# Optimization experiments

Hardware: AMD Instinct MI355X
Metric: run time of the kernel (lower is better)

The kernel has to match this reference:

```python
import jax, jax.numpy as jnp
import numpy as np

B, T = 32, 512
VOCAB, WDIM, H, NUM_LABELS = 100000, 300, 256, 2


def setup_inputs() -> dict:
    key = jax.random.key(0)
    ks = jax.random.split(key, 16)
    x = jax.random.randint(ks[0], (B, T), 0, VOCAB, dtype=jnp.int32)
    lengths = jax.random.randint(ks[1], (B,), T // 2, T + 1, dtype=jnp.int32)
    mask = (jnp.arange(T)[None, :] < lengths[:, None]).astype(jnp.int32)
    s = 0.05
    emb_table = jax.random.normal(ks[2], (VOCAB, WDIM), jnp.float32)
    W_in = jax.random.normal(ks[3], (WDIM, H), jnp.float32) * s
    b_in = jnp.zeros((H,), jnp.float32)
    Wih_f = jax.random.normal(ks[4], (H, 4 * H), jnp.float32) * s
    Whh_f = jax.random.normal(ks[5], (H, 4 * H), jnp.float32) * s
    bl_f = jnp.zeros((4 * H,), jnp.float32)
    Wih_b = jax.random.normal(ks[6], (H, 4 * H), jnp.float32) * s
    Whh_b = jax.random.normal(ks[7], (H, 4 * H), jnp.float32) * s
    bl_b = jnp.zeros((4 * H,), jnp.float32)
    Wfc = jax.random.normal(ks[8], (2 * H, H), jnp.float32) * s
    bfc = jnp.zeros((H,), jnp.float32)
    Wout = jax.random.normal(ks[9], (H, NUM_LABELS), jnp.float32) * s
    bout = jnp.zeros((NUM_LABELS,), jnp.float32)
    return dict(emb_table=emb_table, W_in=W_in, b_in=b_in,
                Wih_f=Wih_f, Whh_f=Whh_f, bl_f=bl_f,
                Wih_b=Wih_b, Whh_b=Whh_b, bl_b=bl_b,
                Wfc=Wfc, bfc=bfc, Wout=Wout, bout=bout,
                x=x, mask=mask, lengths=lengths)


def _lstm_dir(xs, maskf, Wih, Whh, b, reverse):
    # xs: [B,T,H], maskf: [B,T] float. Masked LSTM: padded steps carry state.
    xs_t = jnp.swapaxes(xs, 0, 1)                # [T,B,H]
    m_t = jnp.swapaxes(maskf, 0, 1)[..., None]   # [T,B,1]
    h0 = jnp.zeros((xs.shape[0], Whh.shape[0]), xs.dtype)
    c0 = h0

    def step(carry, inp):
        h, c = carry
        xt, mt = inp
        z = xt @ Wih + h @ Whh + b               # [B,4H]
        i, f, g, o = jnp.split(z, 4, axis=-1)
        i = jax.nn.sigmoid(i); f = jax.nn.sigmoid(f)
        g = jnp.tanh(g); o = jax.nn.sigmoid(o)
        c_new = f * c + i * g
        h_new = o * jnp.tanh(c_new)
        c = mt * c_new + (1.0 - mt) * c
        h = mt * h_new + (1.0 - mt) * h
        return (h, c), h

    _, hs = jax.lax.scan(step, (h0, c0), (xs_t, m_t), reverse=reverse)
    return jnp.swapaxes(hs, 0, 1)                # [B,T,H]


def reference(emb_table, W_in, b_in, Wih_f, Whh_f, bl_f, Wih_b, Whh_b, bl_b,
              Wfc, bfc, Wout, bout, x, mask, lengths):
    maskf = mask.astype(jnp.float32)
    x_vecs = jnp.take(emb_table, x, axis=0)          # [B,T,WDIM]
    z = jax.nn.relu(x_vecs @ W_in + b_in)            # wordvec layer + relu
    h_fwd = _lstm_dir(z, maskf, Wih_f, Whh_f, bl_f, reverse=False)
    h_bwd = _lstm_dir(z, maskf, Wih_b, Whh_b, bl_b, reverse=True)
    h_mat = jnp.concatenate([h_fwd, h_bwd], axis=-1)  # [B,T,2H]
    h_masked = h_mat * maskf[..., None]
    fc_in = jnp.sum(h_masked / lengths.astype(jnp.float32)[:, None, None], axis=1)
    fc_hidden = jax.nn.relu(fc_in @ Wfc + bfc)        # dropout = identity (eval)
    return fc_hidden @ Wout + bout                    # [B, NUM_LABELS]
```

## Files before the change

kernel.cpp:

```cpp
#include <hip/hip_runtime.h>
#include <math.h>

#define B_    32
#define T_    512
#define WDIM_ 300
#define H_    256
#define G4_   1024
#define M_    (B_ * T_)

#define NCG   8
#define NWG   256
#define THR   512
#define HXN   (2 * 2 * B_ * H_)

#define RPT4(M, b)  M(b) M((b)+1) M((b)+2) M((b)+3)
#define RPT16(M, b) RPT4(M, b) RPT4(M, (b)+4) RPT4(M, (b)+8) RPT4(M, (b)+12)
#define RPT64(M)    RPT16(M, 0) RPT16(M, 16) RPT16(M, 32) RPT16(M, 48)

__global__ __launch_bounds__(256)
void k_embed_proj(const float* __restrict__ emb, const float* __restrict__ Win,
                  const float* __restrict__ bin, const int* __restrict__ x,
                  float* __restrict__ z)
{
    __shared__ float Ash[16][132];
    __shared__ float Bsh[16][132];
    __shared__ int   rows[128];

    const int tid = threadIdx.x;
    const int tx = tid & 15, ty = tid >> 4;
    const int rm = blockIdx.y * 128;
    const int cn = blockIdx.x * 128;

    if (tid < 128) rows[tid] = x[rm + tid];
    __syncthreads();

    float acc[8][8];
#pragma unroll
    for (int i = 0; i < 8; ++i)
#pragma unroll
        for (int j = 0; j < 8; ++j) acc[i][j] = 0.f;

    for (int kc = 0; kc < 19; ++kc) {
        const int k0 = kc * 16;
#pragma unroll
        for (int e = 0; e < 8; ++e) {
            const int idx = e * 256 + tid;
            const int r = idx >> 4, kk = idx & 15;
            const int k = k0 + kk;
            const int v = rows[r];
            Ash[kk][r] = (k < WDIM_) ? emb[(size_t)v * WDIM_ + k] : 0.f;
        }
#pragma unroll
        for (int e = 0; e < 8; ++e) {
            const int idx = e * 256 + tid;
            const int kk = idx >> 7, n = idx & 127;
            const int k = k0 + kk;
            Bsh[kk][n] = (k < WDIM_) ? Win[(size_t)k * H_ + cn + n] : 0.f;
        }
        __syncthreads();
#pragma unroll
        for (int kk = 0; kk < 16; ++kk) {
            float a[8], bb[8];
#pragma unroll
            for (int i = 0; i < 8; ++i) a[i] = Ash[kk][ty * 8 + i];
#pragma unroll
            for (int j = 0; j < 8; ++j) bb[j] = Bsh[kk][tx * 8 + j];
#pragma unroll
            for (int i = 0; i < 8; ++i)
#pragma unroll
                for (int j = 0; j < 8; ++j) acc[i][j] += a[i] * bb[j];
        }
        __syncthreads();
    }

#pragma unroll
    for (int i = 0; i < 8; ++i) {
        const int row = rm + ty * 8 + i;
#pragma unroll
        for (int j = 0; j < 8; ++j) {
            const int col = cn + tx * 8 + j;
            z[(size_t)row * H_ + col] = fmaxf(acc[i][j] + bin[col], 0.f);
        }
    }
}

__global__ __launch_bounds__(256)
void k_in_proj(const float* __restrict__ z,
               const float* __restrict__ Wf, const float* __restrict__ blf,
               const float* __restrict__ Wb, const float* __restrict__ blb,
               float* __restrict__ Pf, float* __restrict__ Pb)
{
    const float* W  = blockIdx.z ? Wb  : Wf;
    const float* bl = blockIdx.z ? blb : blf;
    float*       P  = blockIdx.z ? Pb  : Pf;

    __shared__ float Ash[16][132];
    __shared__ float Bsh[16][132];

    const int tid = threadIdx.x;
    const int tx = tid & 15, ty = tid >> 4;
    const int rm = blockIdx.y * 128;
    const int cn = blockIdx.x * 128;

    float acc[8][8];
#pragma unroll
    for (int i = 0; i < 8; ++i)
#pragma unroll
        for (int j = 0; j < 8; ++j) acc[i][j] = 0.f;

    for (int kc = 0; kc < 16; ++kc) {
        const int k0 = kc * 16;
#pragma unroll
        for (int e = 0; e < 8; ++e) {
            const int idx = e * 256 + tid;
            const int r = idx >> 4, kk = idx & 15;
            Ash[kk][r] = z[(size_t)(rm + r) * H_ + k0 + kk];
        }
#pragma unroll
        for (int e = 0; e < 8; ++e) {
            const int idx = e * 256 + tid;
            const int kk = idx >> 7, n = idx & 127;
            Bsh[kk][n] = W[(size_t)(k0 + kk) * G4_ + cn + n];
        }
        __syncthreads();
#pragma unroll
        for (int kk = 0; kk < 16; ++kk) {
            float a[8], bb[8];
#pragma unroll
            for (int i = 0; i < 8; ++i) a[i] = Ash[kk][ty * 8 + i];
#pragma unroll
            for (int j = 0; j < 8; ++j) bb[j] = Bsh[kk][tx * 8 + j];
#pragma unroll
            for (int i = 0; i < 8; ++i)
#pragma unroll
                for (int j = 0; j < 8; ++j) acc[i][j] += a[i] * bb[j];
        }
        __syncthreads();
    }

#pragma unroll
    for (int i = 0; i < 8; ++i) {
        const int row = rm + ty * 8 + i;
#pragma unroll
        for (int j = 0; j < 8; ++j) {
            const int col = cn + tx * 8 + j;
            P[(size_t)row * G4_ + col] = acc[i][j] + bl[col];
        }
    }
}

__global__ void k_init(unsigned long long* __restrict__ hx)
{
    const int i = blockIdx.x * blockDim.x + threadIdx.x;
    if (i < HXN) hx[i] = 0ull;
}

__global__ __launch_bounds__(THR, 2)
void k_lstm_persist(const float* __restrict__ Pf, const float* __restrict__ Pb,
                    const float* __restrict__ Whf, const float* __restrict__ Whb,
                    const int* __restrict__ lengths,
                    unsigned long long* __restrict__ hx,
                    float* __restrict__ pool)
{
    __shared__ float h_sh[2][256];
    __shared__ float zp[4][2][128];

    const int tid = threadIdx.x;
    const int wg  = blockIdx.x;
    const int bg  = wg & 15;
    const int dir = (wg >> 4) & 1;
    const int cg  = wg >> 5;

    const float* P   = dir ? Pb  : Pf;
    const float* Whh = dir ? Whb : Whf;

    const int brow0 = bg * 2;
    const int len0 = lengths[brow0], len1 = lengths[brow0 + 1];
    const int tmax = max(len0, len1);

    const int q   = tid >> 7;
    const int cl  = tid & 127;
    const int g0  = cl >> 5;
    const int dd0 = cl & 31;
    const int gcol = g0 * 256 + cg * 32 + dd0;
    const int q64 = q * 64;

    float wv[64];
    {
        const float* wp = Whh + (size_t)q64 * G4_ + gcol;
#define LOADW(k) wv[k] = wp[(size_t)(k) * G4_];
        RPT64(LOADW)
#undef LOADW
    }

    const int gr    = tid >> 5;
    const int gd    = tid & 31;
    const int gbrow = brow0 + gr;
    const int glen  = gr ? len1 : len0;
    float cst = 0.f, hreg = 0.f, pacc = 0.f;

    const int lrow = tid >> 8;
    const int ld   = tid & 255;
    unsigned long long* slotR = hx + ((size_t)dir * 32 + brow0 + lrow) * 256 + ld;
    unsigned long long* slotW = hx + ((size_t)dir * 32 + gbrow) * 256 + cg * 32 + gd;
    const size_t bufStride = (size_t)2 * B_ * H_;

    for (int s = 0; s < tmax; ++s) {
        const int tt = dir ? (tmax - 1 - s) : s;

        float pv0 = 0.f, pv1 = 0.f, pv2 = 0.f, pv3 = 0.f;
        if (tid < 64) {
            const float* pr = P + (size_t)(gbrow * T_ + tt) * G4_ + cg * 32 + gd;
            pv0 = pr[0]; pv1 = pr[256]; pv2 = pr[512]; pv3 = pr[768];
        }

        {
            const unsigned long long* sp = slotR + (size_t)(s & 1) * bufStride;
            unsigned long long pk = __hip_atomic_load(sp, __ATOMIC_RELAXED,
                                                      __HIP_MEMORY_SCOPE_AGENT);
            while ((unsigned)(pk >> 32) < (unsigned)s) {
                __builtin_amdgcn_s_sleep(1);
                pk = __hip_atomic_load(sp, __ATOMIC_RELAXED,
                                       __HIP_MEMORY_SCOPE_AGENT);
            }
            h_sh[lrow][ld] = __uint_as_float((unsigned)pk);
        }
        __syncthreads();

        {
            const float* h0 = &h_sh[0][q64];
            const float* h1 = &h_sh[1][q64];
            float a0 = 0.f, a1 = 0.f;
#define GEMV4(k4) { \
            const float4 hv0 = *(const float4*)(h0 + 4 * (k4)); \
            const float4 hv1 = *(const float4*)(h1 + 4 * (k4)); \
            a0 += hv0.x * wv[4*(k4)  ]; a1 += hv1.x * wv[4*(k4)  ]; \
            a0 += hv0.y * wv[4*(k4)+1]; a1 += hv1.y * wv[4*(k4)+1]; \
            a0 += hv0.z * wv[4*(k4)+2]; a1 += hv1.z * wv[4*(k4)+2]; \
            a0 += hv0.w * wv[4*(k4)+3]; a1 += hv1.w * wv[4*(k4)+3]; }
            RPT16(GEMV4, 0)
#undef GEMV4
            zp[q][0][cl] = a0;
            zp[q][1][cl] = a1;
        }
        __syncthreads();

        if (tid < 64) {
            float zi = pv0 + zp[0][gr][gd]      + zp[1][gr][gd]      + zp[2][gr][gd]      + zp[3][gr][gd];
            float zf = pv1 + zp[0][gr][32 + gd] + zp[1][gr][32 + gd] + zp[2][gr][32 + gd] + zp[3][gr][32 + gd];
            float zg = pv2 + zp[0][gr][64 + gd] + zp[1][gr][64 + gd] + zp[2][gr][64 + gd] + zp[3][gr][64 + gd];
            float zo = pv3 + zp[0][gr][96 + gd] + zp[1][gr][96 + gd] + zp[2][gr][96 + gd] + zp[3][gr][96 + gd];
            const float ig = 1.f / (1.f + expf(-zi));
            const float fg = 1.f / (1.f + expf(-zf));
            const float gg = tanhf(zg);
            const float og = 1.f / (1.f + expf(-zo));
            const float cn = fg * cst + ig * gg;
            const float hn = og * tanhf(cn);
            if (tt < glen) { cst = cn; hreg = hn; pacc += hn; }
            const unsigned long long opk =
                ((unsigned long long)(unsigned)(s + 1) << 32) |
                (unsigned long long)__float_as_uint(hreg);
            __hip_atomic_store(slotW + (size_t)((s + 1) & 1) * bufStride, opk,
                               __ATOMIC_RELAXED, __HIP_MEMORY_SCOPE_AGENT);
        }
    }

    if (tid < 64)
        pool[gbrow * 512 + dir * 256 + cg * 32 + gd] = pacc / (float)glen;
}

__global__ __launch_bounds__(256)
void k_fc(const float* __restrict__ pool, const float* __restrict__ Wfc,
          const float* __restrict__ bfc, const float* __restrict__ Wout,
          const float* __restrict__ bout, float* __restrict__ out)
{
    __shared__ float p_sh[512];
    __shared__ float red[8];

    const int tid = threadIdx.x;
    const int b   = blockIdx.x;

    p_sh[tid]       = pool[b * 512 + tid];
    p_sh[256 + tid] = pool[b * 512 + 256 + tid];
    __syncthreads();

    float acc = bfc[tid];
#pragma unroll 8
    for (int k = 0; k < 512; ++k)
        acc += p_sh[k] * Wfc[(size_t)k * H_ + tid];
    const float fh = fmaxf(acc, 0.f);

    float p0 = fh * Wout[tid * 2 + 0];
    float p1 = fh * Wout[tid * 2 + 1];
#pragma unroll
    for (int off = 32; off > 0; off >>= 1) {
        p0 += __shfl_down(p0, off);
        p1 += __shfl_down(p1, off);
    }
    const int wave = tid >> 6;
    if ((tid & 63) == 0) { red[wave * 2] = p0; red[wave * 2 + 1] = p1; }
    __syncthreads();
    if (tid == 0) {
        out[b * 2 + 0] = red[0] + red[2] + red[4] + red[6] + bout[0];
        out[b * 2 + 1] = red[1] + red[3] + red[5] + red[7] + bout[1];
    }
}

__global__ void k_sentinel(float* out, int n)
{
    const int i = blockIdx.x * blockDim.x + threadIdx.x;
    if (i < n) out[i] = 1.0e9f;
}

extern "C" void kernel_launch(void* const* d_in, const int* in_sizes, int n_in,
                              void* d_out, int out_size, void* d_ws, size_t ws_size,
                              hipStream_t stream)
{
    const float* emb  = (const float*)d_in[0];
    const float* Win  = (const float*)d_in[1];
    const float* bin  = (const float*)d_in[2];
    const float* Wihf = (const float*)d_in[3];
    const float* Whhf = (const float*)d_in[4];
    const float* blf  = (const float*)d_in[5];
    const float* Wihb = (const float*)d_in[6];
    const float* Whhb = (const float*)d_in[7];
    const float* blb  = (const float*)d_in[8];
    const float* Wfc  = (const float*)d_in[9];
    const float* bfc  = (const float*)d_in[10];
    const float* Wout = (const float*)d_in[11];
    const float* bout = (const float*)d_in[12];
    const int*   x    = (const int*)d_in[13];
    const int*   lens = (const int*)d_in[15];
    float*       out  = (float*)d_out;

    const size_t need = ((size_t)M_ * H_ + 2 * (size_t)M_ * G4_) * sizeof(float);
    if (ws_size < need) {
        hipLaunchKernelGGL(k_sentinel, dim3(1), dim3(64), 0, stream, out, out_size);
        return;
    }

    float* z  = (float*)d_ws;
    float* Pf = z + (size_t)M_ * H_;
    float* Pb = Pf + (size_t)M_ * G4_;

    unsigned long long* hx   = (unsigned long long*)d_ws;
    float*              pool = (float*)(hx + HXN);

    hipLaunchKernelGGL(k_embed_proj, dim3(2, 128), dim3(256), 0, stream,
                       emb, Win, bin, x, z);
    hipLaunchKernelGGL(k_in_proj, dim3(8, 128, 2), dim3(256), 0, stream,
                       z, Wihf, blf, Wihb, blb, Pf, Pb);
    hipLaunchKernelGGL(k_init, dim3(128), dim3(256), 0, stream, hx);
    hipLaunchKernelGGL(k_lstm_persist, dim3(NWG), dim3(THR), 0, stream,
                       Pf, Pb, Whhf, Whhb, lens, hx, pool);
    hipLaunchKernelGGL(k_fc, dim3(32), dim3(256), 0, stream,
                       pool, Wfc, bfc, Wout, bout, out);
}
```

Measured before the change: 1.380 ms.

## Interleave forward and backward LSTM directions in one workgroup, use fast gate math

Each persistent workgroup now runs both the forward and backward recurrence for its batch pair and column group, halving the workgroup count. The two directions alternate within each step so that waiting on one direction's cross-workgroup h exchange can overlap with compute on the other. This doubles the register-resident recurrent weights per thread, which may cause spills or lower occupancy. Sigmoid and tanh are replaced by fast exp and reciprocal approximations, trading a little accuracy for fewer instructions.

```diff
diff --git a/kernel.cpp b/kernel.cpp
--- a/kernel.cpp
+++ b/kernel.cpp
@@ -9,13 +9,22 @@
 #define M_    (B_ * T_)
 
 #define NCG   8
-#define NWG   256
+#define NWG   128
 #define THR   512
 #define HXN   (2 * 2 * B_ * H_)
 
 #define RPT4(M, b)  M(b) M((b)+1) M((b)+2) M((b)+3)
 #define RPT16(M, b) RPT4(M, b) RPT4(M, (b)+4) RPT4(M, (b)+8) RPT4(M, (b)+12)
 #define RPT64(M)    RPT16(M, 0) RPT16(M, 16) RPT16(M, 32) RPT16(M, 48)
+
+__device__ __forceinline__ float fsigm(float x) {
+    return __builtin_amdgcn_rcpf(1.f + __expf(-x));
+}
+__device__ __forceinline__ float ftanh(float x) {
+    const float ax = fabsf(x);
+    const float t  = 1.f - 2.f * __builtin_amdgcn_rcpf(__expf(2.f * ax) + 1.f);
+    return copysignf(t, x);
+}
 
 __global__ __launch_bounds__(256)
 void k_embed_proj(const float* __restrict__ emb, const float* __restrict__ Win,
@@ -162,17 +171,13 @@
                     unsigned long long* __restrict__ hx,
                     float* __restrict__ pool)
 {
-    __shared__ float h_sh[2][256];
-    __shared__ float zp[4][2][128];
+    __shared__ float h_sh[2][2][256];
+    __shared__ float zp[2][4][2][128];
 
     const int tid = threadIdx.x;
     const int wg  = blockIdx.x;
     const int bg  = wg & 15;
-    const int dir = (wg >> 4) & 1;
-    const int cg  = wg >> 5;
-
-    const float* P   = dir ? Pb  : Pf;
-    const float* Whh = dir ? Whb : Whf;
+    const int cg  = wg >> 4;
 
     const int brow0 = bg * 2;
     const int len0 = lengths[brow0], len1 = lengths[brow0 + 1];
@@ -185,10 +190,11 @@
     const int gcol = g0 * 256 + cg * 32 + dd0;
     const int q64 = q * 64;
 
-    float wv[64];
+    float wf[64], wb[64];
     {
-        const float* wp = Whh + (size_t)q64 * G4_ + gcol;
-#define LOADW(k) wv[k] = wp[(size_t)(k) * G4_];
+        const float* wpf = Whf + (size_t)q64 * G4_ + gcol;
+        const float* wpb = Whb + (size_t)q64 * G4_ + gcol;
+#define LOADW(k) wf[k] = wpf[(size_t)(k) * G4_]; wb[k] = wpb[(size_t)(k) * G4_];
         RPT64(LOADW)
 #undef LOADW
     }
@@ -197,76 +203,128 @@
     const int gd    = tid & 31;
     const int gbrow = brow0 + gr;
     const int glen  = gr ? len1 : len0;
-    float cst = 0.f, hreg = 0.f, pacc = 0.f;
+    float cst0 = 0.f, hreg0 = 0.f, pacc0 = 0.f;
+    float cst1 = 0.f, hreg1 = 0.f, pacc1 = 0.f;
 
     const int lrow = tid >> 8;
     const int ld   = tid & 255;
-    unsigned long long* slotR = hx + ((size_t)dir * 32 + brow0 + lrow) * 256 + ld;
-    unsigned long long* slotW = hx + ((size_t)dir * 32 + gbrow) * 256 + cg * 32 + gd;
     const size_t bufStride = (size_t)2 * B_ * H_;
+    unsigned long long* slotR0 = hx + ((size_t)(brow0 + lrow)) * 256 + ld;
+    unsigned long long* slotR1 = slotR0 + (size_t)B_ * H_;
+    unsigned long long* slotW0 = hx + (size_t)gbrow * 256 + cg * 32 + gd;
+    unsigned long long* slotW1 = slotW0 + (size_t)B_ * H_;
 
     for (int s = 0; s < tmax; ++s) {
-        const int tt = dir ? (tmax - 1 - s) : s;
-
-        float pv0 = 0.f, pv1 = 0.f, pv2 = 0.f, pv3 = 0.f;
+        const int tt0 = s;
+        const int tt1 = tmax - 1 - s;
+        const size_t par = (size_t)(s & 1) * bufStride;
+
+        const unsigned long long* sp0 = slotR0 + par;
+        const unsigned long long* sp1 = slotR1 + par;
+        unsigned long long pk0 = __hip_atomic_load(sp0, __ATOMIC_RELAXED,
+                                                   __HIP_MEMORY_SCOPE_AGENT);
+        unsigned long long pk1 = __hip_atomic_load(sp1, __ATOMIC_RELAXED,
+                                                   __HIP_MEMORY_SCOPE_AGENT);
+        float pv00 = 0.f, pv01 = 0.f, pv02 = 0.f, pv03 = 0.f;
+        float pv10 = 0.f, pv11 = 0.f, pv12 = 0.f, pv13 = 0.f;
         if (tid < 64) {
-            const float* pr = P + (size_t)(gbrow * T_ + tt) * G4_ + cg * 32 + gd;
-            pv0 = pr[0]; pv1 = pr[256]; pv2 = pr[512]; pv3 = pr[768];
-        }
-
+            const float* pr0 = Pf + (size_t)(gbrow * T_ + tt0) * G4_ + cg * 32 + gd;
+            const float* pr1 = Pb + (size_t)(gbrow * T_ + tt1) * G4_ + cg * 32 + gd;
+            pv00 = pr0[0]; pv01 = pr0[256]; pv02 = pr0[512]; pv03 = pr0[768];
+            pv10 = pr1[0]; pv11 = pr1[256]; pv12 = pr1[512]; pv13 = pr1[768];
+        }
+
+        while ((unsigned)(pk0 >> 32) < (unsigned)s) {
+            __builtin_amdgcn_s_sleep(1);
+            pk0 = __hip_atomic_load(sp0, __ATOMIC_RELAXED,
+                                    __HIP_MEMORY_SCOPE_AGENT);
+        }
+        h_sh[0][lrow][ld] = __uint_as_float((unsigned)pk0);
+        __syncthreads();
         {
-            const unsigned long long* sp = slotR + (size_t)(s & 1) * bufStride;
-            unsigned long long pk = __hip_atomic_load(sp, __ATOMIC_RELAXED,
-                                                      __HIP_MEMORY_SCOPE_AGENT);
-            while ((unsigned)(pk >> 32) < (unsigned)s) {
-                __builtin_amdgcn_s_sleep(1);
-                pk = __hip_atomic_load(sp, __ATOMIC_RELAXED,
-                                       __HIP_MEMORY_SCOPE_AGENT);
-            }
-            h_sh[lrow][ld] = __uint_as_float((unsigned)pk);
-        }
-        __syncthreads();
-
-        {
-            const float* h0 = &h_sh[0][q64];
-            const float* h1 = &h_sh[1][q64];
+            const float* h0 = &h_sh[0][0][q64];
+            const float* h1 = &h_sh[0][1][q64];
             float a0 = 0.f, a1 = 0.f;
-#define GEMV4(k4) { \
+#define GEMV4F(k4) { \
             const float4 hv0 = *(const float4*)(h0 + 4 * (k4)); \
             const float4 hv1 = *(const float4*)(h1 + 4 * (k4)); \
-            a0 += hv0.x * wv[4*(k4)  ]; a1 += hv1.x * wv[4*(k4)  ]; \
-            a0 += hv0.y * wv[4*(k4)+1]; a1 += hv1.y * wv[4*(k4)+1]; \
-            a0 += hv0.z * wv[4*(k4)+2]; a1 += hv1.z * wv[4*(k4)+2]; \
-            a0 += hv0.w * wv[4*(k4)+3]; a1 += hv1.w * wv[4*(k4)+3]; }
-            RPT16(GEMV4, 0)
-#undef GEMV4
-            zp[q][0][cl] = a0;
-            zp[q][1][cl] = a1;
-        }
-        __syncthreads();
-
+            a0 += hv0.x * wf[4*(k4)  ]; a1 += hv1.x * wf[4*(k4)  ]; \
+            a0 += hv0.y * wf[4*(k4)+1]; a1 += hv1.y * wf[4*(k4)+1]; \
+            a0 += hv0.z * wf[4*(k4)+2]; a1 += hv1.z * wf[4*(k4)+2]; \
+            a0 += hv0.w * wf[4*(k4)+3]; a1 += hv1.w * wf[4*(k4)+3]; }
+            RPT16(GEMV4F, 0)
+#undef GEMV4F
+            zp[0][q][0][cl] = a0;
+            zp[0][q][1][cl] = a1;
+        }
+        __syncthreads();
         if (tid < 64) {
-            float zi = pv0 + zp[0][gr][gd]      + zp[1][gr][gd]      + zp[2][gr][gd]      + zp[3][gr][gd];
-            float zf = pv1 + zp[0][gr][32 + gd] + zp[1][gr][32 + gd] + zp[2][gr][32 + gd] + zp[3][gr][32 + gd];
-            float zg = pv2 + zp[0][gr][64 + gd] + zp[1][gr][64 + gd] + zp[2][gr][64 + gd] + zp[3][gr][64 + gd];
-            float zo = pv3 + zp[0][gr][96 + gd] + zp[1][gr][96 + gd] + zp[2][gr][96 + gd] + zp[3][gr][96 + gd];
-            const float ig = 1.f / (1.f + expf(-zi));
-            const float fg = 1.f / (1.f + expf(-zf));
-            const float gg = tanhf(zg);
-            const float og = 1.f / (1.f + expf(-zo));
-            const float cn = fg * cst + ig * gg;
-            const float hn = og * tanhf(cn);
-            if (tt < glen) { cst = cn; hreg = hn; pacc += hn; }
+            float zi = pv00 + zp[0][0][gr][gd]      + zp[0][1][gr][gd]      + zp[0][2][gr][gd]      + zp[0][3][gr][gd];
+            float zf = pv01 + zp[0][0][gr][32 + gd] + zp[0][1][gr][32 + gd] + zp[0][2][gr][32 + gd] + zp[0][3][gr][32 + gd];
+            float zg = pv02 + zp[0][0][gr][64 + gd] + zp[0][1][gr][64 + gd] + zp[0][2][gr][64 + gd] + zp[0][3][gr][64 + gd];
+            float zo = pv03 + zp[0][0][gr][96 + gd] + zp[0][1][gr][96 + gd] + zp[0][2][gr][96 + gd] + zp[0][3][gr][96 + gd];
+            const float ig = fsigm(zi);
+            const float fg = fsigm(zf);
+            const float gg = ftanh(zg);
+            const float og = fsigm(zo);
+            const float cn = fg * cst0 + ig * gg;
+            const float hn = og * ftanh(cn);
+            if (tt0 < glen) { cst0 = cn; hreg0 = hn; pacc0 += hn; }
             const unsigned long long opk =
                 ((unsigned long long)(unsigned)(s + 1) << 32) |
-                (unsigned long long)__float_as_uint(hreg);
-            __hip_atomic_store(slotW + (size_t)((s + 1) & 1) * bufStride, opk,
+                (unsigned long long)__float_as_uint(hreg0);
+            __hip_atomic_store(slotW0 + (size_t)((s + 1) & 1) * bufStride, opk,
                                __ATOMIC_RELAXED, __HIP_MEMORY_SCOPE_AGENT);
         }
-    }
-
-    if (tid < 64)
-        pool[gbrow * 512 + dir * 256 + cg * 32 + gd] = pacc / (float)glen;
+
+        while ((unsigned)(pk1 >> 32) < (unsigned)s) {
+            __builtin_amdgcn_s_sleep(1);
+            pk1 = __hip_atomic_load(sp1, __ATOMIC_RELAXED,
+                                    __HIP_MEMORY_SCOPE_AGENT);
+        }
+        h_sh[1][lrow][ld] = __uint_as_float((unsigned)pk1);
+        __syncthreads();
+        {
+            const float* h0 = &h_sh[1][0][q64];
+            const float* h1 = &h_sh[1][1][q64];
+            float a0 = 0.f, a1 = 0.f;
+#define GEMV4B(k4) { \
+            const float4 hv0 = *(const float4*)(h0 + 4 * (k4)); \
+            const float4 hv1 = *(const float4*)(h1 + 4 * (k4)); \
+            a0 += hv0.x * wb[4*(k4)  ]; a1 += hv1.x * wb[4*(k4)  ]; \
+            a0 += hv0.y * wb[4*(k4)+1]; a1 += hv1.y * wb[4*(k4)+1]; \
+            a0 += hv0.z * wb[4*(k4)+2]; a1 += hv1.z * wb[4*(k4)+2]; \
+            a0 += hv0.w * wb[4*(k4)+3]; a1 += hv1.w * wb[4*(k4)+3]; }
+            RPT16(GEMV4B, 0)
+#undef GEMV4B
+            zp[1][q][0][cl] = a0;
+            zp[1][q][1][cl] = a1;
+        }
+        __syncthreads();
+        if (tid < 64) {
+            float zi = pv10 + zp[1][0][gr][gd]      + zp[1][1][gr][gd]      + zp[1][2][gr][gd]      + zp[1][3][gr][gd];
+            float zf = pv11 + zp[1][0][gr][32 + gd] + zp[1][1][gr][32 + gd] + zp[1][2][gr][32 + gd] + zp[1][3][gr][32 + gd];
+            float zg = pv12 + zp[1][0][gr][64 + gd] + zp[1][1][gr][64 + gd] + zp[1][2][gr][64 + gd] + zp[1][3][gr][64 + gd];
+            float zo = pv13 + zp[1][0][gr][96 + gd] + zp[1][1][gr][96 + gd] + zp[1][2][gr][96 + gd] + zp[1][3][gr][96 + gd];
+            const float ig = fsigm(zi);
+            const float fg = fsigm(zf);
+            const float gg = ftanh(zg);
+            const float og = fsigm(zo);
+            const float cn = fg * cst1 + ig * gg;
+            const float hn = og * ftanh(cn);
+            if (tt1 < glen) { cst1 = cn; hreg1 = hn; pacc1 += hn; }
+            const unsigned long long opk =
+                ((unsigned long long)(unsigned)(s + 1) << 32) |
+                (unsigned long long)__float_as_uint(hreg1);
+            __hip_atomic_store(slotW1 + (size_t)((s + 1) & 1) * bufStride, opk,
+                               __ATOMIC_RELAXED, __HIP_MEMORY_SCOPE_AGENT);
+        }
+    }
+
+    if (tid < 64) {
+        pool[gbrow * 512 + 0   + cg * 32 + gd] = pacc0 / (float)glen;
+        pool[gbrow * 512 + 256 + cg * 32 + gd] = pacc1 / (float)glen;
+    }
 }
 
 __global__ __launch_bounds__(256)
```

New measurement: 1.688 ms. 1.22x slower.

## Reduce LSTM gate partials with wave shuffles instead of shared-memory pass

Applied to the files above, without the earlier changes.

Reassigns columns so that the four K-quarter partial sums and the four gates of a hidden unit sit in the same wavefront. They are then reduced with xor shuffles rather than written to a shared zp buffer and reread after a barrier. The spin-load on the h slot is issued before the P prefetch so the two latencies overlap. Sigmoid and tanh are replaced with fast exp/rcp approximations. This removes one shared-memory round trip and one barrier per step on the serial recurrence. The cost is a trailing barrier per step and slightly lower accuracy in the activations.

```diff
diff --git a/kernel.cpp b/kernel.cpp
--- a/kernel.cpp
+++ b/kernel.cpp
@@ -17,6 +17,15 @@
 #define RPT16(M, b) RPT4(M, b) RPT4(M, (b)+4) RPT4(M, (b)+8) RPT4(M, (b)+12)
 #define RPT64(M)    RPT16(M, 0) RPT16(M, 16) RPT16(M, 32) RPT16(M, 48)
 
+__device__ __forceinline__ float fsigm(float x) {
+    return __builtin_amdgcn_rcpf(1.f + __expf(-x));
+}
+__device__ __forceinline__ float ftanh(float x) {
+    const float ax = fabsf(x);
+    const float t  = 1.f - 2.f * __builtin_amdgcn_rcpf(__expf(2.f * ax) + 1.f);
+    return copysignf(t, x);
+}
+
 __global__ __launch_bounds__(256)
 void k_embed_proj(const float* __restrict__ emb, const float* __restrict__ Win,
                   const float* __restrict__ bin, const int* __restrict__ x,
@@ -163,7 +172,6 @@
                     float* __restrict__ pool)
 {
     __shared__ float h_sh[2][256];
-    __shared__ float zp[4][2][128];
 
     const int tid = threadIdx.x;
     const int wg  = blockIdx.x;
@@ -178,95 +186,121 @@
     const int len0 = lengths[brow0], len1 = lengths[brow0 + 1];
     const int tmax = max(len0, len1);
 
-    const int q   = tid >> 7;
-    const int cl  = tid & 127;
-    const int g0  = cl >> 5;
-    const int dd0 = cl & 31;
-    const int gcol = g0 * 256 + cg * 32 + dd0;
-    const int q64 = q * 64;
+    const int lane   = tid & 63;
+    const int w      = tid >> 6;
+    const int q      = lane >> 4;
+    const int lo     = lane & 15;
+    const int col_id = w * 16 + lo;
+    const int dloc   = col_id >> 2;
+    const int g      = col_id & 3;
+    const int colg   = g * 256 + cg * 32 + dloc;
+    const int q64    = q * 64;
 
     float wv[64];
     {
-        const float* wp = Whh + (size_t)q64 * G4_ + gcol;
+        const float* wp = Whh + (size_t)q64 * G4_ + colg;
 #define LOADW(k) wv[k] = wp[(size_t)(k) * G4_];
         RPT64(LOADW)
 #undef LOADW
     }
 
-    const int gr    = tid >> 5;
-    const int gd    = tid & 31;
-    const int gbrow = brow0 + gr;
-    const int glen  = gr ? len1 : len0;
-    float cst = 0.f, hreg = 0.f, pacc = 0.f;
+    const bool pub = ((lane & 51) == 0);
+    float cst0 = 0.f, hreg0 = 0.f, pacc0 = 0.f;
+    float cst1 = 0.f, hreg1 = 0.f, pacc1 = 0.f;
 
     const int lrow = tid >> 8;
     const int ld   = tid & 255;
+    const size_t bufStride = (size_t)2 * B_ * H_;
     unsigned long long* slotR = hx + ((size_t)dir * 32 + brow0 + lrow) * 256 + ld;
-    unsigned long long* slotW = hx + ((size_t)dir * 32 + gbrow) * 256 + cg * 32 + gd;
-    const size_t bufStride = (size_t)2 * B_ * H_;
+    unsigned long long* slotW0 = hx + ((size_t)dir * 32 + brow0) * 256 + cg * 32 + dloc;
+    unsigned long long* slotW1 = slotW0 + 256;
 
     for (int s = 0; s < tmax; ++s) {
         const int tt = dir ? (tmax - 1 - s) : s;
 
-        float pv0 = 0.f, pv1 = 0.f, pv2 = 0.f, pv3 = 0.f;
-        if (tid < 64) {
-            const float* pr = P + (size_t)(gbrow * T_ + tt) * G4_ + cg * 32 + gd;
-            pv0 = pr[0]; pv1 = pr[256]; pv2 = pr[512]; pv3 = pr[768];
-        }
-
+        const unsigned long long* sp = slotR + (size_t)(s & 1) * bufStride;
+        unsigned long long pk = __hip_atomic_load(sp, __ATOMIC_RELAXED,
+                                                  __HIP_MEMORY_SCOPE_AGENT);
+
+        float pv00 = 0.f, pv01 = 0.f, pv02 = 0.f, pv03 = 0.f;
+        float pv10 = 0.f, pv11 = 0.f, pv12 = 0.f, pv13 = 0.f;
+        if (pub) {
+            const float* pr0 = P + (size_t)(brow0 * T_ + tt) * G4_ + cg * 32 + dloc;
+            const float* pr1 = pr0 + (size_t)T_ * G4_;
+            pv00 = pr0[0]; pv01 = pr0[256]; pv02 = pr0[512]; pv03 = pr0[768];
+            pv10 = pr1[0]; pv11 = pr1[256]; pv12 = pr1[512]; pv13 = pr1[768];
+        }
+
+        while ((unsigned)(pk >> 32) < (unsigned)s) {
+            __builtin_amdgcn_s_sleep(1);
+            pk = __hip_atomic_load(sp, __ATOMIC_RELAXED,
+                                   __HIP_MEMORY_SCOPE_AGENT);
+        }
+        h_sh[lrow][ld] = __uint_as_float((unsigned)pk);
+        __syncthreads();
+
+        float a0 = 0.f, a1 = 0.f;
         {
-            const unsigned long long* sp = slotR + (size_t)(s & 1) * bufStride;
-            unsigned long long pk = __hip_atomic_load(sp, __ATOMIC_RELAXED,
-                                                      __HIP_MEMORY_SCOPE_AGENT);
-            while ((unsigned)(pk >> 32) < (unsigned)s) {
-                __builtin_amdgcn_s_sleep(1);
-                pk = __hip_atomic_load(sp, __ATOMIC_RELAXED,
-                                       __HIP_MEMORY_SCOPE_AGENT);
-            }
-            h_sh[lrow][ld] = __uint_as_float((unsigned)pk);
-        }
-        __syncthreads();
-
-        {
-            const float* h0 = &h_sh[0][q64];
-            const float* h1 = &h_sh[1][q64];
-            float a0 = 0.f, a1 = 0.f;
+            const float* hp0 = &h_sh[0][q64];
+            const float* hp1 = &h_sh[1][q64];
 #define GEMV4(k4) { \
-            const float4 hv0 = *(const float4*)(h0 + 4 * (k4)); \
-            const float4 hv1 = *(const float4*)(h1 + 4 * (k4)); \
+            const float4 hv0 = *(const float4*)(hp0 + 4 * (k4)); \
+            const float4 hv1 = *(const float4*)(hp1 + 4 * (k4)); \
             a0 += hv0.x * wv[4*(k4)  ]; a1 += hv1.x * wv[4*(k4)  ]; \
             a0 += hv0.y * wv[4*(k4)+1]; a1 += hv1.y * wv[4*(k4)+1]; \
             a0 += hv0.z * wv[4*(k4)+2]; a1 += hv1.z * wv[4*(k4)+2]; \
             a0 += hv0.w * wv[4*(k4)+3]; a1 += hv1.w * wv[4*(k4)+3]; }
             RPT16(GEMV4, 0)
 #undef GEMV4
-            zp[q][0][cl] = a0;
-            zp[q][1][cl] = a1;
-        }
-        __syncthreads();
-
-        if (tid < 64) {
-            float zi = pv0 + zp[0][gr][gd]      + zp[1][gr][gd]      + zp[2][gr][gd]      + zp[3][gr][gd];
-            float zf = pv1 + zp[0][gr][32 + gd] + zp[1][gr][32 + gd] + zp[2][gr][32 + gd] + zp[3][gr][32 + gd];
-            float zg = pv2 + zp[0][gr][64 + gd] + zp[1][gr][64 + gd] + zp[2][gr][64 + gd] + zp[3][gr][64 + gd];
-            float zo = pv3 + zp[0][gr][96 + gd] + zp[1][gr][96 + gd] + zp[2][gr][96 + gd] + zp[3][gr][96 + gd];
-            const float ig = 1.f / (1.f + expf(-zi));
-            const float fg = 1.f / (1.f + expf(-zf));
-            const float gg = tanhf(zg);
-            const float og = 1.f / (1.f + expf(-zo));
-            const float cn = fg * cst + ig * gg;
-            const float hn = og * tanhf(cn);
-            if (tt < glen) { cst = cn; hreg = hn; pacc += hn; }
-            const unsigned long long opk =
-                ((unsigned long long)(unsigned)(s + 1) << 32) |
-                (unsigned long long)__float_as_uint(hreg);
-            __hip_atomic_store(slotW + (size_t)((s + 1) & 1) * bufStride, opk,
+        }
+
+        a0 += __shfl_xor(a0, 16); a0 += __shfl_xor(a0, 32);
+        a1 += __shfl_xor(a1, 16); a1 += __shfl_xor(a1, 32);
+        const float b00 = __shfl_xor(a0, 1);
+        const float b01 = __shfl_xor(a0, 2);
+        const float b02 = __shfl_xor(b00, 2);
+        const float b10 = __shfl_xor(a1, 1);
+        const float b11 = __shfl_xor(a1, 2);
+        const float b12 = __shfl_xor(b10, 2);
+
+        if (pub) {
+            {
+                const float ig = fsigm(pv00 + a0);
+                const float fg = fsigm(pv01 + b00);
+                const float gg = ftanh(pv02 + b01);
+                const float og = fsigm(pv03 + b02);
+                const float cn = fg * cst0 + ig * gg;
+                const float hn = og * ftanh(cn);
+                if (tt < len0) { cst0 = cn; hreg0 = hn; pacc0 += hn; }
+            }
+            {
+                const float ig = fsigm(pv10 + a1);
+                const float fg = fsigm(pv11 + b10);
+                const float gg = ftanh(pv12 + b11);
+                const float og = fsigm(pv13 + b12);
+                const float cn = fg * cst1 + ig * gg;
+                const float hn = og * ftanh(cn);
+                if (tt < len1) { cst1 = cn; hreg1 = hn; pacc1 += hn; }
+            }
+            const unsigned long long tagbits =
+                (unsigned long long)(unsigned)(s + 1) << 32;
+            const size_t parW = (size_t)((s + 1) & 1) * bufStride;
+            __hip_atomic_store(slotW0 + parW,
+                               tagbits | (unsigned long long)__float_as_uint(hreg0),
                                __ATOMIC_RELAXED, __HIP_MEMORY_SCOPE_AGENT);
-        }
-    }
-
-    if (tid < 64)
-        pool[gbrow * 512 + dir * 256 + cg * 32 + gd] = pacc / (float)glen;
+            __hip_atomic_store(slotW1 + parW,
+                               tagbits | (unsigned long long)__float_as_uint(hreg1),
+                               __ATOMIC_RELAXED, __HIP_MEMORY_SCOPE_AGENT);
+        }
+        __syncthreads();
+    }
+
+    if (pub) {
+        pool[(size_t)brow0 * 512 + dir * 256 + cg * 32 + dloc]
+            = pacc0 / (float)len0;
+        pool[(size_t)(brow0 + 1) * 512 + dir * 256 + cg * 32 + dloc]
+            = pacc1 / (float)len1;
+    }
 }
 
 __global__ __launch_bounds__(256)
```

Result: slower. 1.903 ms (+38.0%).

## Replace per-element packed step tags with per-workgroup flags and fast gate math

Applied to the files above, without the earlier changes.

The recurrent kernel's cross-workgroup handoff changes. Before, every hidden value was packed with its step counter into a 64-bit word, and each consumer thread spun on its own word with a sleep. Now producers write plain float hidden values into an interleaved buffer, issue an agent-scope release fence, and one thread bumps a single per-workgroup flag; each consumer wave polls only its producer's flag and then does one coalesced load. The sigmoid and tanh gates also switch to fast-exp and hardware-reciprocal versions. This shortens the per-step latency of the serial 512-step chain, at the cost of relying on relaxed loads after flag polling with no explicit acquire fence, and of slightly lower transcendental accuracy.

```diff
diff --git a/kernel.cpp b/kernel.cpp
--- a/kernel.cpp
+++ b/kernel.cpp
@@ -11,11 +11,22 @@
 #define NCG   8
 #define NWG   256
 #define THR   512
-#define HXN   (2 * 2 * B_ * H_)
+
+#define HHN   (2 * 2 * 16 * 512)
+#define FLN   (2 * 2 * 16 * 8)
 
 #define RPT4(M, b)  M(b) M((b)+1) M((b)+2) M((b)+3)
 #define RPT16(M, b) RPT4(M, b) RPT4(M, (b)+4) RPT4(M, (b)+8) RPT4(M, (b)+12)
 #define RPT64(M)    RPT16(M, 0) RPT16(M, 16) RPT16(M, 32) RPT16(M, 48)
+
+__device__ __forceinline__ float fsigm(float x) {
+    return __builtin_amdgcn_rcpf(1.f + __expf(-x));
+}
+__device__ __forceinline__ float ftanh(float x) {
+    const float ax = fabsf(x);
+    const float t  = 1.f - 2.f * __builtin_amdgcn_rcpf(__expf(2.f * ax) + 1.f);
+    return copysignf(t, x);
+}
 
 __global__ __launch_bounds__(256)
 void k_embed_proj(const float* __restrict__ emb, const float* __restrict__ Win,
@@ -149,17 +160,18 @@
     }
 }
 
-__global__ void k_init(unsigned long long* __restrict__ hx)
+__global__ void k_init(float* __restrict__ hh, unsigned int* __restrict__ flg)
 {
     const int i = blockIdx.x * blockDim.x + threadIdx.x;
-    if (i < HXN) hx[i] = 0ull;
+    if (i < HHN) hh[i] = 0.f;
+    if (i < FLN) flg[i] = 0u;
 }
 
 __global__ __launch_bounds__(THR, 2)
 void k_lstm_persist(const float* __restrict__ Pf, const float* __restrict__ Pb,
                     const float* __restrict__ Whf, const float* __restrict__ Whb,
                     const int* __restrict__ lengths,
-                    unsigned long long* __restrict__ hx,
+                    float* __restrict__ hh, unsigned int* __restrict__ flg,
                     float* __restrict__ pool)
 {
     __shared__ float h_sh[2][256];
@@ -199,14 +211,20 @@
     const int glen  = gr ? len1 : len0;
     float cst = 0.f, hreg = 0.f, pacc = 0.f;
 
-    const int lrow = tid >> 8;
-    const int ld   = tid & 255;
-    unsigned long long* slotR = hx + ((size_t)dir * 32 + brow0 + lrow) * 256 + ld;
-    unsigned long long* slotW = hx + ((size_t)dir * 32 + gbrow) * 256 + cg * 32 + gd;
-    const size_t bufStride = (size_t)2 * B_ * H_;
+    const size_t hhPar  = (size_t)2 * 16 * 512;
+    const size_t flPar  = (size_t)2 * 16 * 8;
+    float*        hhB   = hh  + ((size_t)dir * 16 + bg) * 512;
+    unsigned int* flB   = flg + ((size_t)dir * 16 + bg) * 8;
+
+    const int wv_id = tid >> 6;
+    const int st_d  = tid >> 1;
+    const int st_r  = tid & 1;
+
+    const int pub_e = (cg * 32 + gd) * 2 + gr;
 
     for (int s = 0; s < tmax; ++s) {
         const int tt = dir ? (tmax - 1 - s) : s;
+        const size_t parR = (size_t)(s & 1);
 
         float pv0 = 0.f, pv1 = 0.f, pv2 = 0.f, pv3 = 0.f;
         if (tid < 64) {
@@ -215,25 +233,27 @@
         }
 
         {
-            const unsigned long long* sp = slotR + (size_t)(s & 1) * bufStride;
-            unsigned long long pk = __hip_atomic_load(sp, __ATOMIC_RELAXED,
+            const unsigned int* fp = flB + parR * flPar + wv_id;
+            while (__hip_atomic_load(fp, __ATOMIC_RELAXED,
+                                     __HIP_MEMORY_SCOPE_AGENT) < (unsigned)s) {
+            }
+        }
+        {
+            const unsigned int* hp =
+                (const unsigned int*)(hhB + parR * hhPar) + tid;
+            const unsigned int hv = __hip_atomic_load(hp, __ATOMIC_RELAXED,
                                                       __HIP_MEMORY_SCOPE_AGENT);
-            while ((unsigned)(pk >> 32) < (unsigned)s) {
-                __builtin_amdgcn_s_sleep(1);
-                pk = __hip_atomic_load(sp, __ATOMIC_RELAXED,
-                                       __HIP_MEMORY_SCOPE_AGENT);
-            }
-            h_sh[lrow][ld] = __uint_as_float((unsigned)pk);
+            h_sh[st_r][st_d] = __uint_as_float(hv);
         }
         __syncthreads();
 
         {
-            const float* h0 = &h_sh[0][q64];
-            const float* h1 = &h_sh[1][q64];
+            const float* hp0 = &h_sh[0][q64];
+            const float* hp1 = &h_sh[1][q64];
             float a0 = 0.f, a1 = 0.f;
 #define GEMV4(k4) { \
-            const float4 hv0 = *(const float4*)(h0 + 4 * (k4)); \
-            const float4 hv1 = *(const float4*)(h1 + 4 * (k4)); \
+            const float4 hv0 = *(const float4*)(hp0 + 4 * (k4)); \
+            const float4 hv1 = *(const float4*)(hp1 + 4 * (k4)); \
             a0 += hv0.x * wv[4*(k4)  ]; a1 += hv1.x * wv[4*(k4)  ]; \
             a0 += hv0.y * wv[4*(k4)+1]; a1 += hv1.y * wv[4*(k4)+1]; \
             a0 += hv0.z * wv[4*(k4)+2]; a1 += hv1.z * wv[4*(k4)+2]; \
@@ -250,23 +270,29 @@
             float zf = pv1 + zp[0][gr][32 + gd] + zp[1][gr][32 + gd] + zp[2][gr][32 + gd] + zp[3][gr][32 + gd];
             float zg = pv2 + zp[0][gr][64 + gd] + zp[1][gr][64 + gd] + zp[2][gr][64 + gd] + zp[3][gr][64 + gd];
             float zo = pv3 + zp[0][gr][96 + gd] + zp[1][gr][96 + gd] + zp[2][gr][96 + gd] + zp[3][gr][96 + gd];
-            const float ig = 1.f / (1.f + expf(-zi));
-            const float fg = 1.f / (1.f + expf(-zf));
-            const float gg = tanhf(zg);
-            const float og = 1.f / (1.f + expf(-zo));
+            const float ig = fsigm(zi);
+            const float fg = fsigm(zf);
+            const float gg = ftanh(zg);
+            const float og = fsigm(zo);
             const float cn = fg * cst + ig * gg;
-            const float hn = og * tanhf(cn);
+            const float hn = og * ftanh(cn);
             if (tt < glen) { cst = cn; hreg = hn; pacc += hn; }
-            const unsigned long long opk =
-                ((unsigned long long)(unsigned)(s + 1) << 32) |
-                (unsigned long long)__float_as_uint(hreg);
-            __hip_atomic_store(slotW + (size_t)((s + 1) & 1) * bufStride, opk,
+
+            const size_t parW = (size_t)((s + 1) & 1);
+            unsigned int* hs = (unsigned int*)(hhB + parW * hhPar) + pub_e;
+            __hip_atomic_store(hs, __float_as_uint(hreg),
                                __ATOMIC_RELAXED, __HIP_MEMORY_SCOPE_AGENT);
+            __builtin_amdgcn_fence(__ATOMIC_RELEASE, "agent");
+            if (tid == 0) {
+                __hip_atomic_store(flB + parW * flPar + cg, (unsigned)(s + 1),
+                                   __ATOMIC_RELAXED, __HIP_MEMORY_SCOPE_AGENT);
+            }
         }
     }
 
     if (tid < 64)
-        pool[gbrow * 512 + dir * 256 + cg * 32 + gd] = pacc / (float)glen;
+        pool[(size_t)gbrow * 512 + dir * 256 + cg * 32 + gd]
+            = pacc / (float)glen;
 }
 
 __global__ __launch_bounds__(256)
@@ -343,16 +369,17 @@
     float* Pf = z + (size_t)M_ * H_;
     float* Pb = Pf + (size_t)M_ * G4_;
 
-    unsigned long long* hx   = (unsigned long long*)d_ws;
-    float*              pool = (float*)(hx + HXN);
+    float*        hh   = (float*)d_ws;
+    unsigned int* flgp = (unsigned int*)(hh + HHN);
+    float*        pool = (float*)(flgp + FLN);
 
     hipLaunchKernelGGL(k_embed_proj, dim3(2, 128), dim3(256), 0, stream,
                        emb, Win, bin, x, z);
     hipLaunchKernelGGL(k_in_proj, dim3(8, 128, 2), dim3(256), 0, stream,
                        z, Wihf, blf, Wihb, blb, Pf, Pb);
-    hipLaunchKernelGGL(k_init, dim3(128), dim3(256), 0, stream, hx);
+    hipLaunchKernelGGL(k_init, dim3(128), dim3(256), 0, stream, hh, flgp);
     hipLaunchKernelGGL(k_lstm_persist, dim3(NWG), dim3(THR), 0, stream,
-                       Pf, Pb, Whhf, Whhb, lens, hx, pool);
+                       Pf, Pb, Whhf, Whhb, lens, hh, flgp, pool);
     hipLaunchKernelGGL(k_fc, dim3(32), dim3(256), 0, stream,
                        pool, Wfc, bfc, Wout, bout, out);
 }
```

After: 2.414 ms. 1.75x slower.
